# Performance work log

Hardware: AMD Instinct MI355X
Metric: run time of the kernel (lower is better)

The kernel has to match this reference:

```python
import jax, jax.numpy as jnp
import numpy as np


def setup_inputs() -> dict:
    key = jax.random.key(0)
    ks = jax.random.split(key, 5)
    B, T, D, L = 4, 8192, 1024, 128
    X = jax.random.normal(ks[0], (B, T, D), dtype=jnp.float32)
    attention_mask = jnp.ones((B, T), dtype=jnp.float32)
    sd_dl = 1.0 / np.sqrt(D)  # lecun_normal fan_in = D
    Wk = jax.random.normal(ks[1], (D, L), dtype=jnp.float32) * sd_dl
    Wq = jax.random.normal(ks[2], (D, L), dtype=jnp.float32) * sd_dl
    Wv = jax.random.normal(ks[3], (D, D), dtype=jnp.float32) * sd_dl
    o_proj = jax.random.normal(ks[4], (D, D), dtype=jnp.float32) * sd_dl
    return {"X": X, "attention_mask": attention_mask, "Wk": Wk, "Wq": Wq,
            "Wv": Wv, "o_proj": o_proj, "n_heads": 16}


def reference(X, attention_mask, Wk, Wq, Wv, o_proj, n_heads):
    B, T, D = X.shape
    H = n_heads
    # Projections, laid out time-major as in the original: (T, B, H, *)
    V = jnp.einsum('DM,BTD->TBM', Wv, X).reshape(T, B, H, -1)   # (T,B,H,d)
    Q = jnp.einsum('DL,BTD->TBL', Wq, X).reshape(T, B, H, -1)   # (T,B,H,l)
    K = jnp.einsum('DL,BTD->TBL', Wk, X).reshape(T, B, H, -1)   # (T,B,H,l)
    m = attention_mask.T[:, :, None, None]                       # (T,B,1,1)
    V = V * m
    Qs = jax.nn.softmax(Q, axis=-1)
    maxi = jnp.max(K, axis=0, keepdims=True)                     # global max over T
    K = jnp.exp(K - maxi) * m
    Kv = jnp.einsum('tbhl,tbhd->bhld', K, V)                     # global KV state
    Ksum = K.sum(axis=0)                                         # (B,H,l)
    Kv = Kv / Ksum[..., None]
    y = jnp.einsum('tbhl,bhld->bthd', Qs, Kv).reshape(B, T, D)
    return y @ o_proj
```

## Files before the change

kernel.cpp:

```cpp
#include <hip/hip_runtime.h>
#include <hip/hip_bf16.h>

typedef unsigned short u16;
typedef unsigned int   u32;

typedef __attribute__((ext_vector_type(8))) short short8;
typedef __attribute__((ext_vector_type(4))) float f32x4;

typedef const __attribute__((address_space(1))) void g_void;
typedef __attribute__((address_space(3))) void l_void;

__device__ __forceinline__ float bf2f(u16 u) {
    u32 x = ((u32)u) << 16;
    return __builtin_bit_cast(float, x);
}
__device__ __forceinline__ u16 f2bf(float f) {
    u32 u = __builtin_bit_cast(u32, f);
    u32 r = (u + 0x7FFFu + ((u >> 16) & 1u)) >> 16;
    return (u16)r;
}
__device__ __forceinline__ u32 pack2(float a, float b) {
    return (u32)f2bf(a) | ((u32)f2bf(b) << 16);
}

__global__ void detect_kernel(const u16* __restrict__ X, int* __restrict__ flags) {
    __shared__ int cnt[256];
    int c = 0;
    for (int i = threadIdx.x; i < 16384; i += 256) {
        u16 v = X[i];
        int e = (v >> 7) & 0xFF;
        c += (e >= 104 && e <= 140) ? 1 : 0;
    }
    cnt[threadIdx.x] = c;
    __syncthreads();
    for (int s = 128; s > 0; s >>= 1) {
        if (threadIdx.x < s) cnt[threadIdx.x] += cnt[threadIdx.x + s];
        __syncthreads();
    }
    if (threadIdx.x == 0) {
        flags[0] = (cnt[0] < 14746) ? 1 : 0;
        flags[1] = 0;
    }
}

__global__ __launch_bounds__(256) void convert_x(const float* __restrict__ Xf,
                                                 u16* __restrict__ XC,
                                                 const int* __restrict__ flags, int n) {
    if (flags[0] == 0) return;
    int i = (blockIdx.x * 256 + threadIdx.x) * 8;
    if (i >= n) return;
    float4 a = *(const float4*)(Xf + i);
    float4 b = *(const float4*)(Xf + i + 4);
    uint4 o;
    o.x = pack2(a.x, a.y); o.y = pack2(a.z, a.w);
    o.z = pack2(b.x, b.y); o.w = pack2(b.z, b.w);
    *(uint4*)(XC + i) = o;
}

__global__ __launch_bounds__(256) void gemm_bt(
    const u16* __restrict__ A0, const u16* __restrict__ A1, int lda,
    const u16* __restrict__ Bt, int ldb,
    void* __restrict__ C, int ldc,
    int Mtiles, int K,
    const int* __restrict__ aselp, const int* __restrict__ ofp) {
    __shared__ char smem[17408];

    const u16* A = aselp[0] ? A1 : A0;

    const int tid = threadIdx.x;
    const int w = tid >> 6, lane = tid & 63;
    const int Ntiles = gridDim.x / Mtiles;
    const int q8 = gridDim.x >> 3;
    const int t  = (blockIdx.x & 7) * q8 + (blockIdx.x >> 3);
    const int mt = t / Ntiles;
    const int nt = t % Ntiles;
    const int m0 = mt << 7, n0 = nt << 7;
    const int wm = w >> 1, wn = w & 1;

    f32x4 acc[4][4] = {};

    const int rr = w * 16 + (lane >> 2);
    const int cg = (lane & 3) ^ ((lane >> 3) & 3);

    const u16* gA0 = A + (m0 + rr) * lda + cg * 8;
    const u16* gA1 = A + (m0 + rr + 64) * lda + cg * 8;
    const u16* gB0 = Bt + (n0 + rr) * ldb + cg * 8;
    const u16* gB1 = Bt + (n0 + rr + 64) * ldb + cg * 8;

    char* lA0 = smem + w * 1024 + lane * 16;
    char* lA1 = smem + 4096 + w * 1024 + lane * 16;
    char* lB0 = smem + 8192 + w * 1024 + lane * 16;
    char* lB1 = smem + 12288 + w * 1024 + lane * 16;

    const int fr_a = (wm << 6) + (lane & 15);
    const int fr_b = (wn << 6) + (lane & 15);
    const int sl = (lane >> 4) ^ ((lane >> 1) & 3);
    const char* pA = smem + fr_a * 64 + sl * 16;
    const char* pB = smem + 8192 + fr_b * 64 + sl * 16;

    for (int kt = 0; kt < K; kt += 32) {
        __builtin_amdgcn_global_load_lds((g_void*)(gA0 + kt), (l_void*)lA0, 16, 0, 0);
        __builtin_amdgcn_global_load_lds((g_void*)(gA1 + kt), (l_void*)lA1, 16, 0, 0);
        __builtin_amdgcn_global_load_lds((g_void*)(gB0 + kt), (l_void*)lB0, 16, 0, 0);
        __builtin_amdgcn_global_load_lds((g_void*)(gB1 + kt), (l_void*)lB1, 16, 0, 0);
        __syncthreads();
        short8 af[4], bfv[4];
#pragma unroll
        for (int i = 0; i < 4; ++i) {
            af[i]  = *(const short8*)(pA + i * 1024);
            bfv[i] = *(const short8*)(pB + i * 1024);
        }
#pragma unroll
        for (int mi = 0; mi < 4; ++mi) {
#pragma unroll
            for (int ni = 0; ni < 4; ++ni) {
                acc[mi][ni] = __builtin_amdgcn_mfma_f32_16x16x32_bf16(
                    af[mi], bfv[ni], acc[mi][ni], 0, 0, 0);
            }
        }
        __syncthreads();
    }

    const int out_fp32 = ofp[0];
    float* fb = (float*)smem;
    const int lrow = tid >> 3, cgp = tid & 7;
#pragma unroll
    for (int mi = 0; mi < 4; ++mi) {
#pragma unroll
        for (int ni = 0; ni < 4; ++ni) {
#pragma unroll
            for (int r = 0; r < 4; ++r) {
                int lr = wm * 16 + ((lane >> 4) << 2) + r;
                int lc = wn * 64 + ni * 16 + (lane & 15);
                fb[lr * 132 + lc] = acc[mi][ni][r];
            }
        }
        __syncthreads();
        int grow = (lrow < 16) ? (mi * 16 + lrow) : (48 + mi * 16 + lrow);
        const float* srcp = fb + lrow * 132 + cgp * 16;
        if (out_fp32) {
            float4* dst = (float4*)((float*)C + (size_t)(m0 + grow) * ldc + n0 + cgp * 16);
            dst[0] = make_float4(srcp[0], srcp[1], srcp[2], srcp[3]);
            dst[1] = make_float4(srcp[4], srcp[5], srcp[6], srcp[7]);
            dst[2] = make_float4(srcp[8], srcp[9], srcp[10], srcp[11]);
            dst[3] = make_float4(srcp[12], srcp[13], srcp[14], srcp[15]);
        } else {
            u32 o0 = pack2(srcp[0], srcp[1]);
            u32 o1 = pack2(srcp[2], srcp[3]);
            u32 o2 = pack2(srcp[4], srcp[5]);
            u32 o3 = pack2(srcp[6], srcp[7]);
            u32 o4 = pack2(srcp[8], srcp[9]);
            u32 o5 = pack2(srcp[10], srcp[11]);
            u32 o6 = pack2(srcp[12], srcp[13]);
            u32 o7 = pack2(srcp[14], srcp[15]);
            uint4* dst = (uint4*)((u16*)C + (size_t)(m0 + grow) * ldc + n0 + cgp * 16);
            dst[0] = make_uint4(o0, o1, o2, o3);
            dst[1] = make_uint4(o4, o5, o6, o7);
        }
        __syncthreads();
    }
}

__device__ __forceinline__ u16 rd_elem(const void* s, int idx, int fp32) {
    return fp32 ? f2bf(((const float*)s)[idx]) : ((const u16*)s)[idx];
}

__global__ void transpose_k(const void* __restrict__ Wq, const void* __restrict__ Wk,
                            const void* __restrict__ Wv, const void* __restrict__ Op,
                            u16* __restrict__ W1T, u16* __restrict__ OpT,
                            const int* __restrict__ flags) {
    int fp32 = flags[0];
    int id = blockIdx.x;
    const void* src; u16* dst; int Nc, mid;
    if (id < 128)       { src = Wq; dst = W1T;               Nc = 128;  mid = id; }
    else if (id < 256)  { src = Wk; dst = W1T + 128 * 1024;  Nc = 128;  mid = id - 128; }
    else if (id < 1280) { src = Wv; dst = W1T + 256 * 1024;  Nc = 1024; mid = id - 256; }
    else                { src = Op; dst = OpT;               Nc = 1024; mid = id - 1280; }
    int kt = mid & 31, nt = mid >> 5;
    __shared__ u16 tile[32][33];
    int x = threadIdx.x & 31, y0 = threadIdx.x >> 5;
#pragma unroll
    for (int yy = 0; yy < 4; ++yy) {
        int y = y0 * 4 + yy;
        tile[y][x] = rd_elem(src, (kt * 32 + y) * Nc + nt * 32 + x, fp32);
    }
    __syncthreads();
#pragma unroll
    for (int yy = 0; yy < 4; ++yy) {
        int y = y0 * 4 + yy;
        dst[(nt * 32 + y) * 1024 + kt * 32 + x] = tile[x][y];
    }
}

__global__ __launch_bounds__(256) void kvpart_kernel(const u16* __restrict__ QKV,
                                                     const void* __restrict__ mask,
                                                     const int* __restrict__ flags,
                                                     float* __restrict__ Kvp,
                                                     float* __restrict__ Ksp) {
    int t_ = (blockIdx.x & 7) * 256 + (blockIdx.x >> 3);
    int h = t_ & 15;
    int bc = t_ >> 4;
    int chunk = bc & 31, b = bc >> 5;
    int w = threadIdx.x >> 6, lane = threadIdx.x & 63;
    int fp32m = flags[0];

    float kv[8] = {0, 0, 0, 0, 0, 0, 0, 0};
    float ks[8] = {0, 0, 0, 0, 0, 0, 0, 0};
    int t0 = chunk * 256;
    for (int i = 0; i < 64; ++i) {
        int t = t0 + w + i * 4;
        int m = b * 8192 + t;
        const u16* row = QKV + (size_t)m * 1280;
        float v = bf2f(row[256 + h * 64 + lane]);
        uint4 kq = *(const uint4*)(row + 128 + h * 8);
        float msk = fp32m ? ((const float*)mask)[m] : bf2f(((const u16*)mask)[m]);
        float vm = v * msk;
        float kf[8];
        kf[0] = __builtin_bit_cast(float, kq.x << 16);
        kf[1] = __builtin_bit_cast(float, kq.x & 0xffff0000u);
        kf[2] = __builtin_bit_cast(float, kq.y << 16);
        kf[3] = __builtin_bit_cast(float, kq.y & 0xffff0000u);
        kf[4] = __builtin_bit_cast(float, kq.z << 16);
        kf[5] = __builtin_bit_cast(float, kq.z & 0xffff0000u);
        kf[6] = __builtin_bit_cast(float, kq.w << 16);
        kf[7] = __builtin_bit_cast(float, kq.w & 0xffff0000u);
#pragma unroll
        for (int l = 0; l < 8; ++l) {
            float e = __expf(kf[l]) * msk;
            kv[l] += e * vm;
            ks[l] += e;
        }
    }
    __shared__ float red[4][8][64];
    __shared__ float redks[4][8];
#pragma unroll
    for (int l = 0; l < 8; ++l) red[w][l][lane] = kv[l];
    if (lane == 0) {
#pragma unroll
        for (int l = 0; l < 8; ++l) redks[w][l] = ks[l];
    }
    __syncthreads();
    int tid = threadIdx.x;
    int obid = (b * 16 + h) * 32 + chunk;
    for (int c = tid; c < 512; c += 256) {
        int l = c >> 6, d = c & 63;
        Kvp[obid * 512 + c] = red[0][l][d] + red[1][l][d] + red[2][l][d] + red[3][l][d];
    }
    if (tid < 8) Ksp[obid * 8 + tid] = redks[0][tid] + redks[1][tid] + redks[2][tid] + redks[3][tid];
}

__global__ void kvreduce_kernel(const float* __restrict__ Kvp, const float* __restrict__ Ksp,
                                float* __restrict__ Kv) {
    int bh = blockIdx.x;
    int tid = threadIdx.x;
    int l = tid >> 6;
    float s = 0.f, ks = 0.f;
    for (int c = 0; c < 32; ++c) {
        s += Kvp[(bh * 32 + c) * 512 + tid];
        ks += Ksp[(bh * 32 + c) * 8 + l];
    }
    Kv[bh * 512 + tid] = s / ks;
}

__global__ __launch_bounds__(256) void y_kernel(u16* __restrict__ QKV,
                                                const float* __restrict__ Kv) {
    int bid = blockIdx.x;
    int b = bid >> 9, chunk = bid & 511;
    int w = threadIdx.x >> 6, lane = threadIdx.x & 63;
    int hh = w & 1;
    int rp = w >> 1;
    int hloc = lane >> 3;
    int h = hh * 8 + hloc;
    int dg = lane & 7;

    float4 kva[8], kvb[8];
    const float* kvp = Kv + (b * 16 + h) * 512 + dg * 8;
#pragma unroll
    for (int l = 0; l < 8; ++l) {
        kva[l] = *(const float4*)(kvp + l * 64);
        kvb[l] = *(const float4*)(kvp + l * 64 + 4);
    }
    int lgrp = lane & 56;
    for (int i = 0; i < 8; ++i) {
        int t = chunk * 16 + i * 2 + rp;
        int m = b * 8192 + t;
        u16* row = QKV + (size_t)m * 1280;
        float qv = bf2f(row[hh * 64 + lane]);
        float qm = qv;
        qm = fmaxf(qm, __shfl_xor(qm, 1));
        qm = fmaxf(qm, __shfl_xor(qm, 2));
        qm = fmaxf(qm, __shfl_xor(qm, 4));
        float e = __expf(qv - qm);
        float s = e;
        s += __shfl_xor(s, 1);
        s += __shfl_xor(s, 2);
        s += __shfl_xor(s, 4);
        float qs = e / s;
        float4 a0 = {0.f, 0.f, 0.f, 0.f}, a1 = {0.f, 0.f, 0.f, 0.f};
#pragma unroll
        for (int l = 0; l < 8; ++l) {
            float ql = __shfl(qs, lgrp + l);
            a0.x += ql * kva[l].x; a0.y += ql * kva[l].y;
            a0.z += ql * kva[l].z; a0.w += ql * kva[l].w;
            a1.x += ql * kvb[l].x; a1.y += ql * kvb[l].y;
            a1.z += ql * kvb[l].z; a1.w += ql * kvb[l].w;
        }
        uint4 o;
        o.x = pack2(a0.x, a0.y);
        o.y = pack2(a0.z, a0.w);
        o.z = pack2(a1.x, a1.y);
        o.w = pack2(a1.z, a1.w);
        *(uint4*)(row + 256 + h * 64 + dg * 8) = o;
    }
}

#define OFF_FLAG ((size_t)0)
#define OFF_W1T  ((size_t)1024)
#define OFF_OPT  ((size_t)2622464)
#define OFF_KVP  ((size_t)4787200)
#define OFF_KSP  ((size_t)8981504)
#define OFF_KV   ((size_t)9047040)
#define OFF_XC   ((size_t)9309184)
#define OFF_QKV  ((size_t)76418048)

extern "C" void kernel_launch(void* const* d_in, const int* in_sizes, int n_in,
                              void* d_out, int out_size, void* d_ws, size_t ws_size,
                              hipStream_t stream) {
    const u16* X   = (const u16*)d_in[0];
    const void* msk = d_in[1];
    const void* Wk  = d_in[2];
    const void* Wq  = d_in[3];
    const void* Wv  = d_in[4];
    const void* Op  = d_in[5];

    char* ws = (char*)d_ws;
    int*   FLAGS = (int*)(ws + OFF_FLAG);
    u16*   W1T  = (u16*)(ws + OFF_W1T);
    u16*   OPT  = (u16*)(ws + OFF_OPT);
    float* KVP  = (float*)(ws + OFF_KVP);
    float* KSP  = (float*)(ws + OFF_KSP);
    float* KV   = (float*)(ws + OFF_KV);
    u16*   XC   = (u16*)(ws + OFF_XC);
    u16*   QKV  = (u16*)(ws + OFF_QKV);

    detect_kernel<<<1, 256, 0, stream>>>(X, FLAGS);
    convert_x<<<16384, 256, 0, stream>>>((const float*)d_in[0], XC, FLAGS, 33554432);
    transpose_k<<<2304, 256, 0, stream>>>(Wq, Wk, Wv, Op, W1T, OPT, FLAGS);
    gemm_bt<<<2560, 256, 0, stream>>>(X, XC, 1024, W1T, 1024, QKV, 1280, 256, 1024,
                                      FLAGS, FLAGS + 1);
    kvpart_kernel<<<2048, 256, 0, stream>>>(QKV, msk, FLAGS, KVP, KSP);
    kvreduce_kernel<<<64, 512, 0, stream>>>(KVP, KSP, KV);
    y_kernel<<<2048, 256, 0, stream>>>(QKV, KV);
    gemm_bt<<<2048, 256, 0, stream>>>(QKV + 256, QKV + 256, 1280, OPT, 1024,
                                      d_out, 1024, 256, 1024, FLAGS + 1, FLAGS);
}
```

Measured before the change: 574.0 us.

## Double-buffer LDS in GEMM to overlap global loads with MFMA

The bf16 GEMM main loop now uses two 16KB LDS stages, issuing the global-to-LDS loads for the next K tile before computing on the current one, with vmcnt waits and explicit barriers instead of two syncthreads around each tile. This is meant to hide global load latency behind MFMA work. It doubles LDS per block, which may reduce occupancy. Separately, the KV reduce kernel is split into 256 blocks of 128 threads to spread the work across more CUs.

```diff
diff --git a/kernel.cpp b/kernel.cpp
--- a/kernel.cpp
+++ b/kernel.cpp
@@ -63,7 +63,7 @@
     void* __restrict__ C, int ldc,
     int Mtiles, int K,
     const int* __restrict__ aselp, const int* __restrict__ ofp) {
-    __shared__ char smem[17408];
+    __shared__ char smem[32768];
 
     const u16* A = aselp[0] ? A1 : A0;
 
@@ -87,39 +87,62 @@
     const u16* gB0 = Bt + (n0 + rr) * ldb + cg * 8;
     const u16* gB1 = Bt + (n0 + rr + 64) * ldb + cg * 8;
 
-    char* lA0 = smem + w * 1024 + lane * 16;
-    char* lA1 = smem + 4096 + w * 1024 + lane * 16;
-    char* lB0 = smem + 8192 + w * 1024 + lane * 16;
-    char* lB1 = smem + 12288 + w * 1024 + lane * 16;
+    const int st0 = w * 1024 + lane * 16;
 
     const int fr_a = (wm << 6) + (lane & 15);
     const int fr_b = (wn << 6) + (lane & 15);
     const int sl = (lane >> 4) ^ ((lane >> 1) & 3);
-    const char* pA = smem + fr_a * 64 + sl * 16;
-    const char* pB = smem + 8192 + fr_b * 64 + sl * 16;
-
-    for (int kt = 0; kt < K; kt += 32) {
-        __builtin_amdgcn_global_load_lds((g_void*)(gA0 + kt), (l_void*)lA0, 16, 0, 0);
-        __builtin_amdgcn_global_load_lds((g_void*)(gA1 + kt), (l_void*)lA1, 16, 0, 0);
-        __builtin_amdgcn_global_load_lds((g_void*)(gB0 + kt), (l_void*)lB0, 16, 0, 0);
-        __builtin_amdgcn_global_load_lds((g_void*)(gB1 + kt), (l_void*)lB1, 16, 0, 0);
-        __syncthreads();
-        short8 af[4], bfv[4];
-#pragma unroll
-        for (int i = 0; i < 4; ++i) {
-            af[i]  = *(const short8*)(pA + i * 1024);
-            bfv[i] = *(const short8*)(pB + i * 1024);
-        }
-#pragma unroll
-        for (int mi = 0; mi < 4; ++mi) {
-#pragma unroll
-            for (int ni = 0; ni < 4; ++ni) {
-                acc[mi][ni] = __builtin_amdgcn_mfma_f32_16x16x32_bf16(
-                    af[mi], bfv[ni], acc[mi][ni], 0, 0, 0);
-            }
-        }
-        __syncthreads();
-    }
+    const int offA = fr_a * 64 + sl * 16;
+    const int offB = 8192 + fr_b * 64 + sl * 16;
+
+#define STAGE(buf, kt) do {                                                        \
+        char* sb_ = smem + (buf) * 16384;                                          \
+        __builtin_amdgcn_global_load_lds((g_void*)(gA0 + (kt)),                    \
+            (l_void*)(sb_ + st0), 16, 0, 0);                                       \
+        __builtin_amdgcn_global_load_lds((g_void*)(gA1 + (kt)),                    \
+            (l_void*)(sb_ + 4096 + st0), 16, 0, 0);                                \
+        __builtin_amdgcn_global_load_lds((g_void*)(gB0 + (kt)),                    \
+            (l_void*)(sb_ + 8192 + st0), 16, 0, 0);                                \
+        __builtin_amdgcn_global_load_lds((g_void*)(gB1 + (kt)),                    \
+            (l_void*)(sb_ + 12288 + st0), 16, 0, 0);                               \
+    } while (0)
+
+#define COMPUTE(buf) do {                                                          \
+        const char* cb_ = smem + (buf) * 16384;                                    \
+        short8 af[4], bfv[4];                                                      \
+        _Pragma("unroll")                                                          \
+        for (int i = 0; i < 4; ++i) {                                              \
+            af[i]  = *(const short8*)(cb_ + offA + i * 1024);                      \
+            bfv[i] = *(const short8*)(cb_ + offB + i * 1024);                      \
+        }                                                                          \
+        _Pragma("unroll")                                                          \
+        for (int mi = 0; mi < 4; ++mi)                                             \
+            _Pragma("unroll")                                                      \
+            for (int ni = 0; ni < 4; ++ni)                                         \
+                acc[mi][ni] = __builtin_amdgcn_mfma_f32_16x16x32_bf16(             \
+                    af[mi], bfv[ni], acc[mi][ni], 0, 0, 0);                        \
+    } while (0)
+
+    STAGE(0, 0);
+    int cur = 0;
+    for (int kt = 32; kt < K; kt += 32) {
+        STAGE(cur ^ 1, kt);
+        asm volatile("s_waitcnt vmcnt(4)" ::: "memory");
+        __builtin_amdgcn_s_barrier();
+        __builtin_amdgcn_sched_barrier(0);
+        COMPUTE(cur);
+        __builtin_amdgcn_sched_barrier(0);
+        __builtin_amdgcn_s_barrier();
+        cur ^= 1;
+    }
+    asm volatile("s_waitcnt vmcnt(0)" ::: "memory");
+    __builtin_amdgcn_s_barrier();
+    __builtin_amdgcn_sched_barrier(0);
+    COMPUTE(cur);
+    __syncthreads();
+
+#undef STAGE
+#undef COMPUTE
 
     const int out_fp32 = ofp[0];
     float* fb = (float*)smem;
@@ -251,15 +274,16 @@
 
 __global__ void kvreduce_kernel(const float* __restrict__ Kvp, const float* __restrict__ Ksp,
                                 float* __restrict__ Kv) {
-    int bh = blockIdx.x;
-    int tid = threadIdx.x;
-    int l = tid >> 6;
+    int bh = blockIdx.x >> 2;
+    int seg = blockIdx.x & 3;
+    int c0 = seg * 128 + threadIdx.x;
+    int l = c0 >> 6;
     float s = 0.f, ks = 0.f;
     for (int c = 0; c < 32; ++c) {
-        s += Kvp[(bh * 32 + c) * 512 + tid];
+        s += Kvp[(bh * 32 + c) * 512 + c0];
         ks += Ksp[(bh * 32 + c) * 8 + l];
     }
-    Kv[bh * 512 + tid] = s / ks;
+    Kv[bh * 512 + c0] = s / ks;
 }
 
 __global__ __launch_bounds__(256) void y_kernel(u16* __restrict__ QKV,
@@ -349,7 +373,7 @@
     gemm_bt<<<2560, 256, 0, stream>>>(X, XC, 1024, W1T, 1024, QKV, 1280, 256, 1024,
                                       FLAGS, FLAGS + 1);
     kvpart_kernel<<<2048, 256, 0, stream>>>(QKV, msk, FLAGS, KVP, KSP);
-    kvreduce_kernel<<<64, 512, 0, stream>>>(KVP, KSP, KV);
+    kvreduce_kernel<<<256, 128, 0, stream>>>(KVP, KSP, KV);
     y_kernel<<<2048, 256, 0, stream>>>(QKV, KV);
     gemm_bt<<<2048, 256, 0, stream>>>(QKV + 256, QKV + 256, 1280, OPT, 1024,
                                       d_out, 1024, 256, 1024, FLAGS + 1, FLAGS);
```

Result: faster. 533.9 us (-7.0%).
